# Optimization experiments

Hardware: AMD Instinct MI355X
Metric: run time of the kernel (lower is better)

Reference implementation:

```python
import jax, jax.numpy as jnp
import numpy as np

BN_EPS = 1e-5


def conv1x1(x, w, b):
    # x: [B, C, H, W], w: [O, C], b: [O]
    return jnp.einsum('bchw,oc->bohw', x, w) + b[None, :, None, None]


def cca(x, wq, bq, wk, bk, wv, bv, wg, bg):
    # Criss-cross attention block: full HWxHW attention with qk dim = C//8
    B, C, H, W = x.shape
    N = H * W
    q = conv1x1(x, wq, bq).reshape(B, -1, N)   # [B, C//8, N]
    k = conv1x1(x, wk, bk).reshape(B, -1, N)   # [B, C//8, N]
    v = conv1x1(x, wv, bv).reshape(B, C, N)    # [B, C, N]
    att = jax.nn.softmax(jnp.einsum('bdq,bdk->bqk', q, k), axis=-1)  # [B, N, N]
    out = jnp.einsum('bck,bqk->bcq', v, att).reshape(B, C, H, W)
    return x + conv1x1(out, wg, bg)


def setup_inputs() -> dict:
    key = jax.random.key(0)
    ks = iter(jax.random.split(key, 64))

    def rn(shape, s=0.1):
        return jax.random.normal(next(ks), shape, dtype=jnp.float32) * s

    C_IN = [48, 96, 192, 384]
    OC = 8            # hardcoded out_channels in the module
    NOUT = 19         # num_outputs
    LC = OC * 4       # last_inp_channels
    d = {}
    d['x0'] = rn((2, 48, 96, 96), 1.0)
    d['x1'] = rn((2, 96, 48, 48), 1.0)
    d['x2'] = rn((2, 192, 24, 24), 1.0)
    d['x3'] = rn((2, 384, 12, 12), 1.0)
    for i, c in enumerate(C_IN):
        d[f'w{i}'] = rn((OC, c))
        d[f'b{i}'] = rn((OC,))
    # cca3 params are never used by the original forward (it calls cca1 on x_3),
    # so only cca0/cca1/cca2 are materialized.
    for i in range(3):
        d[f'cca{i}_wq'] = rn((OC // 8, OC)); d[f'cca{i}_bq'] = rn((OC // 8,))
        d[f'cca{i}_wk'] = rn((OC // 8, OC)); d[f'cca{i}_bk'] = rn((OC // 8,))
        d[f'cca{i}_wv'] = rn((OC, OC));      d[f'cca{i}_bv'] = rn((OC,))
        d[f'cca{i}_wg'] = rn((OC, OC));      d[f'cca{i}_bg'] = rn((OC,))
    d['wl0'] = rn((LC, LC)); d['bl0'] = rn((LC,))
    d['bn_s'] = jnp.ones((LC,), jnp.float32)
    d['bn_b'] = jnp.zeros((LC,), jnp.float32)
    d['bn_m'] = rn((LC,), 0.01)
    d['bn_v'] = jnp.ones((LC,), jnp.float32)
    d['wl1'] = rn((NOUT, LC)); d['bl1'] = rn((NOUT,))
    return d


def reference(x0, x1, x2, x3, w0, b0, w1, b1, w2, b2, w3, b3,
              cca0_wq, cca0_bq, cca0_wk, cca0_bk, cca0_wv, cca0_bv, cca0_wg, cca0_bg,
              cca1_wq, cca1_bq, cca1_wk, cca1_bk, cca1_wv, cca1_bv, cca1_wg, cca1_bg,
              cca2_wq, cca2_bq, cca2_wk, cca2_bk, cca2_wv, cca2_bv, cca2_wg, cca2_bg,
              wl0, bl0, bn_s, bn_b, bn_m, bn_v, wl1, bl1):
    y0 = cca(conv1x1(x0, w0, b0), cca0_wq, cca0_bq, cca0_wk, cca0_bk, cca0_wv, cca0_bv, cca0_wg, cca0_bg)
    y1 = cca(conv1x1(x1, w1, b1), cca1_wq, cca1_bq, cca1_wk, cca1_bk, cca1_wv, cca1_bv, cca1_wg, cca1_bg)
    y2 = cca(conv1x1(x2, w2, b2), cca2_wq, cca2_bq, cca2_wk, cca2_bk, cca2_wv, cca2_bv, cca2_wg, cca2_bg)
    # NOTE: original torch code applies cca1 (not cca3) to x_3 -- reproduced faithfully.
    y3 = cca(conv1x1(x3, w3, b3), cca1_wq, cca1_bq, cca1_wk, cca1_bk, cca1_wv, cca1_bv, cca1_wg, cca1_bg)

    B, C, H0, W0 = y0.shape

    def up(t):
        # torch F.interpolate(mode='bilinear', align_corners=False) == jax half-pixel bilinear
        return jax.image.resize(t, (t.shape[0], t.shape[1], H0, W0), method='bilinear')

    x = jnp.concatenate([y0, up(y1), up(y2), up(y3)], axis=1)  # [B, 32, H0, W0]
    x = conv1x1(x, wl0, bl0)
    scale = (bn_s / jnp.sqrt(bn_v + BN_EPS))[None, :, None, None]
    x = (x - bn_m[None, :, None, None]) * scale + bn_b[None, :, None, None]
    x = jax.nn.relu(x)
    return conv1x1(x, wl1, bl1)
```

## Files before the change

### kernel.cpp

```cpp
#include <hip/hip_runtime.h>
#include <math.h>

#define LB __launch_bounds__(256)

#define NSLOT 24480
#define MT 28
#define NMOM 252
#define NBLK_Q 540
#define NSLICE 4

typedef float f32x4 __attribute__((ext_vector_type(4)));

struct QkvmArgs {
  const float *x0, *x1, *x2, *x3;
  const float *w0, *w1, *w2, *w3;
  const float *c0, *c1, *c2, *c3;
  const float *wq[4], *bq[4], *wk[4], *bk[4], *wv[4], *bv[4];
  float *P, *Q;
  float *MOMP;
};

template<int CG>
__device__ __forceinline__ void qkvm_body(const QkvmArgs& a, const int scale, const int C,
    const int N, const int slotoff, const int rel,
    const float* __restrict__ xp, const float* __restrict__ wp, const float* __restrict__ bp,
    float* s_w, float* s_sm, float* s_red, float* s_kp, float* s_v) {
  constexpr int PX = 256 / CG;
  const int tid = threadIdx.x;
  const int bpb = N / PX;
  const int b = rel / bpb, blk = rel - b*bpb;
  const int px = tid & (PX - 1), cg = tid / PX;
  const int n = blk*PX + px;
  const float* xb = xp + (size_t)b*C*N + n;
  const int c0 = cg*12;
  float xv[12];
  #pragma unroll
  for (int cc = 0; cc < 12; ++cc) xv[cc] = xb[(size_t)(c0+cc)*N];

  for (int i = tid; i < 8*C; i += 256) { const int c = i >> 3, o = i & 7; s_w[i] = wp[o*C + c]; }
  if (tid >= 128 && tid < 192) { const int t = tid - 128; s_sm[32 + t] = a.wv[scale][(t & 7)*8 + (t >> 3)]; }
  if (tid < 8) {
    s_sm[tid]      = bp[tid];
    s_sm[8 + tid]  = a.wq[scale][tid];
    s_sm[16 + tid] = a.wk[scale][tid];
    s_sm[24 + tid] = a.bv[scale][tid];
  }
  if (tid == 96) { s_sm[96] = a.bq[scale][0]; s_sm[97] = a.bk[scale][0]; }
  __syncthreads();

  float p[8];
  #pragma unroll
  for (int o = 0; o < 8; ++o) p[o] = 0.f;
  #pragma unroll
  for (int cc = 0; cc < 12; ++cc) {
    const float x = xv[cc];
    #pragma unroll
    for (int o = 0; o < 8; ++o) p[o] = fmaf(s_w[(c0+cc)*8+o], x, p[o]);
  }
  f32x4* sp = (f32x4*)&s_red[tid*8];
  sp[0] = (f32x4){p[0], p[1], p[2], p[3]};
  sp[1] = (f32x4){p[4], p[5], p[6], p[7]};
  __syncthreads();

  if (tid < PX) {
    float pc[8];
    #pragma unroll
    for (int o = 0; o < 8; ++o) {
      float s = s_sm[o];
      #pragma unroll
      for (int g = 0; g < CG; ++g) s += s_red[(g*PX + tid)*8 + o];
      pc[o] = s;
    }
    float q = s_sm[96], kv = s_sm[97];
    #pragma unroll
    for (int c = 0; c < 8; ++c) { q = fmaf(s_sm[8+c], pc[c], q); kv = fmaf(s_sm[16+c], pc[c], kv); }
    float v[8];
    #pragma unroll
    for (int o = 0; o < 8; ++o) v[o] = s_sm[24 + o];
    #pragma unroll
    for (int c = 0; c < 8; ++c) {
      const float pcc = pc[c];
      #pragma unroll
      for (int o = 0; o < 8; ++o) v[o] = fmaf(s_sm[32 + c*8 + o], pcc, v[o]);
    }
    const int g = slotoff + b*N + n;
    f32x4* Pp = (f32x4*)&a.P[(size_t)g*8];
    Pp[0] = (f32x4){pc[0], pc[1], pc[2], pc[3]};
    Pp[1] = (f32x4){pc[4], pc[5], pc[6], pc[7]};
    a.Q[g] = q;
    s_kp[tid*MT] = 1.f;
    float pw = 1.f;
    #pragma unroll
    for (int m = 1; m < MT; ++m) { pw *= kv; s_kp[tid*MT + m] = pw; }
    #pragma unroll
    for (int j = 0; j < 8; ++j) s_v[tid*8 + j] = v[j];
  }
  __syncthreads();

  if (tid < NMOM) {
    const int m = tid / 9, j = tid - m*9;
    float acc = 0.f;
    if (j == 0) {
      #pragma unroll 8
      for (int e = 0; e < PX; ++e) acc += s_kp[e*MT + m];
    } else {
      #pragma unroll 8
      for (int e = 0; e < PX; ++e) acc = fmaf(s_kp[e*MT + m], s_v[e*8 + (j-1)], acc);
    }
    a.MOMP[(size_t)blockIdx.x*NMOM + tid] = acc;
  }
}

__global__ LB void qkvm_kernel(QkvmArgs a) {
  __shared__ __align__(16) float s_w[3072];
  __shared__ __align__(16) float s_sm[104];
  __shared__ __align__(16) float s_red[256*8];
  __shared__ __align__(16) float s_kp[64*MT];
  __shared__ __align__(16) float s_v[64*8];
  const int bid = blockIdx.x;
  if (bid < 288)      qkvm_body<4> (a, 0, 48,  9216, 0,     bid,     a.x0, a.w0, a.c0, s_w, s_sm, s_red, s_kp, s_v);
  else if (bid < 432) qkvm_body<8> (a, 1, 96,  2304, 18432, bid-288, a.x1, a.w1, a.c1, s_w, s_sm, s_red, s_kp, s_v);
  else if (bid < 504) qkvm_body<16>(a, 2, 192, 576,  23040, bid-432, a.x2, a.w2, a.c2, s_w, s_sm, s_red, s_kp, s_v);
  else                qkvm_body<32>(a, 3, 384, 144,  24192, bid-504, a.x3, a.w3, a.c3, s_w, s_sm, s_red, s_kp, s_v);
}

__global__ LB void momred_kernel(const float* __restrict__ MOMP, float* __restrict__ MOMQ) {
  const int sb = blockIdx.x / NSLICE, sl = blockIdx.x - sb*NSLICE;
  const int tid = threadIdx.x;
  if (tid >= NMOM) return;
  const int start[8] = {0, 144, 288, 360, 432, 468, 504, 522};
  const int cnt[8]   = {144, 144, 72, 72, 36, 36, 18, 18};
  const int r0 = start[sb] + (cnt[sb]*sl)/NSLICE;
  const int r1 = start[sb] + (cnt[sb]*(sl+1))/NSLICE;
  const float* bp = MOMP + (size_t)r0*NMOM + tid;
  const int c = r1 - r0;
  float a0=0.f,a1=0.f,a2=0.f,a3=0.f,a4=0.f,a5=0.f,a6=0.f,a7=0.f;
  int t = 0;
  for (; t + 8 <= c; t += 8) {
    a0 += bp[(size_t)(t+0)*NMOM];
    a1 += bp[(size_t)(t+1)*NMOM];
    a2 += bp[(size_t)(t+2)*NMOM];
    a3 += bp[(size_t)(t+3)*NMOM];
    a4 += bp[(size_t)(t+4)*NMOM];
    a5 += bp[(size_t)(t+5)*NMOM];
    a6 += bp[(size_t)(t+6)*NMOM];
    a7 += bp[(size_t)(t+7)*NMOM];
  }
  for (; t < c; ++t) a0 += bp[(size_t)t*NMOM];
  const float s = ((a0+a1)+(a2+a3)) + ((a4+a5)+(a6+a7));
  MOMQ[(size_t)blockIdx.x*NMOM + tid] = s;
}

struct FinArgs {
  const float *Q, *P, *MOMQ;
  const float *wg0, *bg0, *wg1, *bg1, *wg2, *bg2;
  float *Y;
};

__global__ LB void finish_kernel(FinArgs a) {
  __shared__ __align__(16) float smom[8*MT*12];
  __shared__ float swg[3][64], sbg[3][8];
  const int tid = threadIdx.x;
  for (int i = tid; i < 8*MT*12; i += 256) smom[i] = 0.f;
  if (tid < 64) { swg[0][tid] = a.wg0[tid]; swg[1][tid] = a.wg1[tid]; swg[2][tid] = a.wg2[tid]; }
  if (tid < 8)  { sbg[0][tid] = a.bg0[tid]; sbg[1][tid] = a.bg1[tid]; sbg[2][tid] = a.bg2[tid]; }
  __syncthreads();
  for (int i = tid; i < 8*NMOM; i += 256) {
    const int sbi = i / NMOM, r = i - sbi*NMOM;
    const int m = r / 9, j = r - m*9;
    const float* qp = a.MOMQ + (size_t)sbi*NSLICE*NMOM + r;
    float s = 0.f;
    #pragma unroll
    for (int sl = 0; sl < NSLICE; ++sl) s += qp[(size_t)sl*NMOM];
    smom[sbi*(MT*12) + m*12 + j] = s;
  }
  __syncthreads();
  const int g = blockIdx.x*256 + tid;
  if (g >= NSLOT) return;
  int scale, N, off, widx;
  if (g < 18432)      { scale=0; N=9216; off=0;     widx=0; }
  else if (g < 23040) { scale=1; N=2304; off=18432; widx=1; }
  else if (g < 24192) { scale=2; N=576;  off=23040; widx=2; }
  else                { scale=3; N=144;  off=24192; widx=1; }
  const int b = (g - off >= N) ? 1 : 0;
  const int sb = scale*2 + b;
  const float q = a.Q[g];
  const float* mb = &smom[sb*(MT*12)];
  float t = 1.f, den = 0.f;
  float num[8];
  #pragma unroll
  for (int c = 0; c < 8; ++c) num[c] = 0.f;
  #pragma unroll
  for (int m = 0; m < MT; ++m) {
    const f32x4 a0 = *(const f32x4*)&mb[m*12];
    const f32x4 a1 = *(const f32x4*)&mb[m*12 + 4];
    const f32x4 a2 = *(const f32x4*)&mb[m*12 + 8];
    den    = fmaf(t, a0.x, den);
    num[0] = fmaf(t, a0.y, num[0]); num[1] = fmaf(t, a0.z, num[1]); num[2] = fmaf(t, a0.w, num[2]);
    num[3] = fmaf(t, a1.x, num[3]); num[4] = fmaf(t, a1.y, num[4]); num[5] = fmaf(t, a1.z, num[5]);
    num[6] = fmaf(t, a1.w, num[6]); num[7] = fmaf(t, a2.x, num[7]);
    if (m + 1 < MT) t *= q * (1.f/(float)(m+1));
  }
  const float inv = 1.f/den;
  float o8[8];
  #pragma unroll
  for (int c = 0; c < 8; ++c) o8[c] = num[c]*inv;
  const f32x4 pA = *(const f32x4*)&a.P[(size_t)g*8];
  const f32x4 pB = *(const f32x4*)&a.P[(size_t)g*8 + 4];
  const float pv[8] = {pA.x, pA.y, pA.z, pA.w, pB.x, pB.y, pB.z, pB.w};
  const float* wg = swg[widx];
  float y[8];
  #pragma unroll
  for (int o = 0; o < 8; ++o) {
    float s2 = pv[o] + sbg[widx][o];
    #pragma unroll
    for (int c = 0; c < 8; ++c) s2 = fmaf(wg[o*8 + c], o8[c], s2);
    y[o] = s2;
  }
  f32x4* Yp = (f32x4*)&a.Y[(size_t)g*8];
  Yp[0] = (f32x4){y[0], y[1], y[2], y[3]};
  Yp[1] = (f32x4){y[4], y[5], y[6], y[7]};
}

template<int HS>
__device__ inline void bilerp8(float* zo, const float* Yb, int h, int w) {
  constexpr float inv = (float)HS/96.0f;
  const float sy = (h + 0.5f)*inv - 0.5f;
  const float sx = (w + 0.5f)*inv - 0.5f;
  const int iy0 = (int)floorf(sy); const float fy = sy - (float)iy0;
  const int ix0 = (int)floorf(sx); const float fx = sx - (float)ix0;
  const int y0 = min(max(iy0, 0), HS-1), y1 = min(max(iy0 + 1, 0), HS-1);
  const int x0 = min(max(ix0, 0), HS-1), x1 = min(max(ix0 + 1, 0), HS-1);
  const float* p00 = &Yb[(size_t)(y0*HS + x0)*8];
  const float* p01 = &Yb[(size_t)(y0*HS + x1)*8];
  const float* p10 = &Yb[(size_t)(y1*HS + x0)*8];
  const float* p11 = &Yb[(size_t)(y1*HS + x1)*8];
  const float w00 = (1.f-fy)*(1.f-fx), w01 = (1.f-fy)*fx, w10 = fy*(1.f-fx), w11 = fy*fx;
  #pragma unroll
  for (int c = 0; c < 8; ++c)
    zo[c] = w00*p00[c] + w01*p01[c] + w10*p10[c] + w11*p11[c];
}

__global__ LB void head_kernel(const float* __restrict__ Y,
                               const float* wl0, const float* bl0,
                               const float* bn_s, const float* bn_b,
                               const float* bn_m, const float* bn_v,
                               const float* wl1, const float* bl1,
                               float* __restrict__ out) {
  __shared__ float s_wl0[1024], s_wl1[608];
  __shared__ float s_bl0[32], s_sc[32], s_sh[32], s_bl1[19];
  const int tid = threadIdx.x;
  for (int i = tid; i < 1024; i += 256) s_wl0[i] = wl0[i];
  for (int i = tid; i < 608;  i += 256) s_wl1[i] = wl1[i];
  if (tid < 32) {
    s_bl0[tid] = bl0[tid];
    const float sc = bn_s[tid] / sqrtf(bn_v[tid] + 1e-5f);
    s_sc[tid] = sc;
    s_sh[tid] = bn_b[tid] - bn_m[tid]*sc;
  }
  if (tid >= 32 && tid < 51) s_bl1[tid - 32] = bl1[tid - 32];
  __syncthreads();
  const int gp = blockIdx.x*256 + tid;
  const int b = (gp >= 9216) ? 1 : 0;
  const int n = gp - b*9216;
  const int h = n / 96, w = n - h*96;
  float z[32];
  {
    const float4 zA = *(const float4*)&Y[(size_t)(b*9216 + n)*8];
    const float4 zB = *(const float4*)&Y[(size_t)(b*9216 + n)*8 + 4];
    z[0]=zA.x; z[1]=zA.y; z[2]=zA.z; z[3]=zA.w; z[4]=zB.x; z[5]=zB.y; z[6]=zB.z; z[7]=zB.w;
  }
  bilerp8<48>(z + 8,  &Y[(size_t)(18432 + b*2304)*8], h, w);
  bilerp8<24>(z + 16, &Y[(size_t)(23040 + b*576)*8],  h, w);
  bilerp8<12>(z + 24, &Y[(size_t)(24192 + b*144)*8],  h, w);
  float o19[19];
  #pragma unroll
  for (int j = 0; j < 19; ++j) o19[j] = s_bl1[j];
  #pragma unroll 1
  for (int o = 0; o < 32; ++o) {
    float sA = s_bl0[o], sB = 0.f;
    #pragma unroll
    for (int c4 = 0; c4 < 4; ++c4) {
      const float4 wv = *(const float4*)&s_wl0[o*32 + c4*4];
      sA = fmaf(wv.x, z[c4*4+0], sA);
      sA = fmaf(wv.y, z[c4*4+1], sA);
      sA = fmaf(wv.z, z[c4*4+2], sA);
      sA = fmaf(wv.w, z[c4*4+3], sA);
    }
    #pragma unroll
    for (int c4 = 4; c4 < 8; ++c4) {
      const float4 wv = *(const float4*)&s_wl0[o*32 + c4*4];
      sB = fmaf(wv.x, z[c4*4+0], sB);
      sB = fmaf(wv.y, z[c4*4+1], sB);
      sB = fmaf(wv.z, z[c4*4+2], sB);
      sB = fmaf(wv.w, z[c4*4+3], sB);
    }
    const float t = fmaxf(fmaf(sA + sB, s_sc[o], s_sh[o]), 0.f);
    #pragma unroll
    for (int j = 0; j < 19; ++j) o19[j] = fmaf(s_wl1[j*32 + o], t, o19[j]);
  }
  #pragma unroll
  for (int j = 0; j < 19; ++j)
    out[((size_t)b*19 + j)*9216 + n] = o19[j];
}

extern "C" void kernel_launch(void* const* d_in, const int* in_sizes, int n_in,
                              void* d_out, int out_size, void* d_ws, size_t ws_size,
                              hipStream_t stream) {
  (void)in_sizes; (void)n_in; (void)out_size; (void)ws_size;
  const float* wq[3]; const float* bq[3]; const float* wk[3]; const float* bk[3];
  const float* wv[3]; const float* bv[3]; const float* wg[3]; const float* bg[3];
  for (int i = 0; i < 3; ++i) {
    const int base = 12 + i*8;
    wq[i] = (const float*)d_in[base + 0]; bq[i] = (const float*)d_in[base + 1];
    wk[i] = (const float*)d_in[base + 2]; bk[i] = (const float*)d_in[base + 3];
    wv[i] = (const float*)d_in[base + 4]; bv[i] = (const float*)d_in[base + 5];
    wg[i] = (const float*)d_in[base + 6]; bg[i] = (const float*)d_in[base + 7];
  }
  const int m4[4] = {0, 1, 2, 1};

  float* ws = (float*)d_ws;
  float* P = ws;
  float* Q = P + (size_t)NSLOT*8;
  float* MOMP = Q + NSLOT;
  float* MOMQ = MOMP + (size_t)NBLK_Q*NMOM;
  float* Y = MOMQ + (size_t)8*NSLICE*NMOM;

  QkvmArgs qa;
  qa.x0 = (const float*)d_in[0]; qa.x1 = (const float*)d_in[1];
  qa.x2 = (const float*)d_in[2]; qa.x3 = (const float*)d_in[3];
  qa.w0 = (const float*)d_in[4];  qa.c0 = (const float*)d_in[5];
  qa.w1 = (const float*)d_in[6];  qa.c1 = (const float*)d_in[7];
  qa.w2 = (const float*)d_in[8];  qa.c2 = (const float*)d_in[9];
  qa.w3 = (const float*)d_in[10]; qa.c3 = (const float*)d_in[11];
  for (int s = 0; s < 4; ++s) {
    qa.wq[s] = wq[m4[s]]; qa.bq[s] = bq[m4[s]];
    qa.wk[s] = wk[m4[s]]; qa.bk[s] = bk[m4[s]];
    qa.wv[s] = wv[m4[s]]; qa.bv[s] = bv[m4[s]];
  }
  qa.P = P; qa.Q = Q; qa.MOMP = MOMP;

  FinArgs fa;
  fa.Q = Q; fa.P = P; fa.MOMQ = MOMQ;
  fa.wg0 = wg[0]; fa.bg0 = bg[0];
  fa.wg1 = wg[1]; fa.bg1 = bg[1];
  fa.wg2 = wg[2]; fa.bg2 = bg[2];
  fa.Y = Y;

  qkvm_kernel<<<NBLK_Q, 256, 0, stream>>>(qa);
  momred_kernel<<<8*NSLICE, 256, 0, stream>>>(MOMP, MOMQ);
  finish_kernel<<<96, 256, 0, stream>>>(fa);
  head_kernel<<<72, 256, 0, stream>>>(Y, (const float*)d_in[36], (const float*)d_in[37],
                                      (const float*)d_in[38], (const float*)d_in[39],
                                      (const float*)d_in[40], (const float*)d_in[41],
                                      (const float*)d_in[42], (const float*)d_in[43],
                                      (float*)d_out);
}
```

Before: 32.39 us.

## Fuse attention finish and head kernels into one row-pair kernel

Merges the finish kernel (Taylor-moment attention evaluation plus gamma conv) and the head kernel (upsample, concat conv, BN, ReLU, output conv) into one launch. Each block handles two output rows of one batch. It recomputes the low-resolution rows it needs for bilinear interpolation into LDS and reads them from there instead of from a global Y buffer. This removes one kernel launch and the Y round trip through global memory. In exchange, the moment reduction and low-res Taylor evaluations are done redundantly across blocks, only 192 of 256 threads do head work, and LDS use per block is larger.

```diff
diff --git a/kernel.cpp b/kernel.cpp
--- a/kernel.cpp
+++ b/kernel.cpp
@@ -151,41 +151,9 @@
   MOMQ[(size_t)blockIdx.x*NMOM + tid] = s;
 }
 
-struct FinArgs {
-  const float *Q, *P, *MOMQ;
-  const float *wg0, *bg0, *wg1, *bg1, *wg2, *bg2;
-  float *Y;
-};
-
-__global__ LB void finish_kernel(FinArgs a) {
-  __shared__ __align__(16) float smom[8*MT*12];
-  __shared__ float swg[3][64], sbg[3][8];
-  const int tid = threadIdx.x;
-  for (int i = tid; i < 8*MT*12; i += 256) smom[i] = 0.f;
-  if (tid < 64) { swg[0][tid] = a.wg0[tid]; swg[1][tid] = a.wg1[tid]; swg[2][tid] = a.wg2[tid]; }
-  if (tid < 8)  { sbg[0][tid] = a.bg0[tid]; sbg[1][tid] = a.bg1[tid]; sbg[2][tid] = a.bg2[tid]; }
-  __syncthreads();
-  for (int i = tid; i < 8*NMOM; i += 256) {
-    const int sbi = i / NMOM, r = i - sbi*NMOM;
-    const int m = r / 9, j = r - m*9;
-    const float* qp = a.MOMQ + (size_t)sbi*NSLICE*NMOM + r;
-    float s = 0.f;
-    #pragma unroll
-    for (int sl = 0; sl < NSLICE; ++sl) s += qp[(size_t)sl*NMOM];
-    smom[sbi*(MT*12) + m*12 + j] = s;
-  }
-  __syncthreads();
-  const int g = blockIdx.x*256 + tid;
-  if (g >= NSLOT) return;
-  int scale, N, off, widx;
-  if (g < 18432)      { scale=0; N=9216; off=0;     widx=0; }
-  else if (g < 23040) { scale=1; N=2304; off=18432; widx=1; }
-  else if (g < 24192) { scale=2; N=576;  off=23040; widx=2; }
-  else                { scale=3; N=144;  off=24192; widx=1; }
-  const int b = (g - off >= N) ? 1 : 0;
-  const int sb = scale*2 + b;
-  const float q = a.Q[g];
-  const float* mb = &smom[sb*(MT*12)];
+__device__ __forceinline__ void taylor_eval(const float* __restrict__ mb, const float* __restrict__ wg,
+                                            const float* __restrict__ bg8, const float q,
+                                            const float* __restrict__ Pp, float* y) {
   float t = 1.f, den = 0.f;
   float num[8];
   #pragma unroll
@@ -205,103 +173,141 @@
   float o8[8];
   #pragma unroll
   for (int c = 0; c < 8; ++c) o8[c] = num[c]*inv;
-  const f32x4 pA = *(const f32x4*)&a.P[(size_t)g*8];
-  const f32x4 pB = *(const f32x4*)&a.P[(size_t)g*8 + 4];
+  const f32x4 pA = *(const f32x4*)Pp;
+  const f32x4 pB = *(const f32x4*)(Pp + 4);
   const float pv[8] = {pA.x, pA.y, pA.z, pA.w, pB.x, pB.y, pB.z, pB.w};
-  const float* wg = swg[widx];
-  float y[8];
   #pragma unroll
   for (int o = 0; o < 8; ++o) {
-    float s2 = pv[o] + sbg[widx][o];
+    float s2 = pv[o] + bg8[o];
     #pragma unroll
     for (int c = 0; c < 8; ++c) s2 = fmaf(wg[o*8 + c], o8[c], s2);
     y[o] = s2;
   }
-  f32x4* Yp = (f32x4*)&a.Y[(size_t)g*8];
-  Yp[0] = (f32x4){y[0], y[1], y[2], y[3]};
-  Yp[1] = (f32x4){y[4], y[5], y[6], y[7]};
 }
 
 template<int HS>
-__device__ inline void bilerp8(float* zo, const float* Yb, int h, int w) {
+__device__ __forceinline__ void bilerp_lds(float* zo, const float* __restrict__ sYb,
+                                           const int r, const int h, const int w) {
   constexpr float inv = (float)HS/96.0f;
   const float sy = (h + 0.5f)*inv - 0.5f;
   const float sx = (w + 0.5f)*inv - 0.5f;
   const int iy0 = (int)floorf(sy); const float fy = sy - (float)iy0;
   const int ix0 = (int)floorf(sx); const float fx = sx - (float)ix0;
-  const int y0 = min(max(iy0, 0), HS-1), y1 = min(max(iy0 + 1, 0), HS-1);
+  const float syE = (2*r + 0.5f)*inv - 0.5f;
+  const int ybase = (int)floorf(syE);
+  const int ly0 = iy0 - ybase;
   const int x0 = min(max(ix0, 0), HS-1), x1 = min(max(ix0 + 1, 0), HS-1);
-  const float* p00 = &Yb[(size_t)(y0*HS + x0)*8];
-  const float* p01 = &Yb[(size_t)(y0*HS + x1)*8];
-  const float* p10 = &Yb[(size_t)(y1*HS + x0)*8];
-  const float* p11 = &Yb[(size_t)(y1*HS + x1)*8];
+  const float* p00 = &sYb[((ly0  )*HS + x0)*8];
+  const float* p01 = &sYb[((ly0  )*HS + x1)*8];
+  const float* p10 = &sYb[((ly0+1)*HS + x0)*8];
+  const float* p11 = &sYb[((ly0+1)*HS + x1)*8];
   const float w00 = (1.f-fy)*(1.f-fx), w01 = (1.f-fy)*fx, w10 = fy*(1.f-fx), w11 = fy*fx;
   #pragma unroll
   for (int c = 0; c < 8; ++c)
     zo[c] = w00*p00[c] + w01*p01[c] + w10*p10[c] + w11*p11[c];
 }
 
-__global__ LB void head_kernel(const float* __restrict__ Y,
-                               const float* wl0, const float* bl0,
-                               const float* bn_s, const float* bn_b,
-                               const float* bn_m, const float* bn_v,
-                               const float* wl1, const float* bl1,
-                               float* __restrict__ out) {
+struct HFArgs {
+  const float *Q, *P, *MOMQ;
+  const float *wg0, *bg0, *wg1, *bg1, *wg2, *bg2;
+  const float *wl0, *bl0, *bn_s, *bn_b, *bn_m, *bn_v, *wl1, *bl1;
+  float *out;
+};
+
+__global__ LB void headfin_kernel(HFArgs a) {
+  __shared__ __align__(16) float smom[8*MT*12];
+  __shared__ __align__(16) float sY[2016];
+  __shared__ float swg[3][64], sbg[3][8];
   __shared__ float s_wl0[1024], s_wl1[608];
   __shared__ float s_bl0[32], s_sc[32], s_sh[32], s_bl1[19];
   const int tid = threadIdx.x;
-  for (int i = tid; i < 1024; i += 256) s_wl0[i] = wl0[i];
-  for (int i = tid; i < 608;  i += 256) s_wl1[i] = wl1[i];
-  if (tid < 32) {
-    s_bl0[tid] = bl0[tid];
-    const float sc = bn_s[tid] / sqrtf(bn_v[tid] + 1e-5f);
-    s_sc[tid] = sc;
-    s_sh[tid] = bn_b[tid] - bn_m[tid]*sc;
-  }
-  if (tid >= 32 && tid < 51) s_bl1[tid - 32] = bl1[tid - 32];
-  __syncthreads();
-  const int gp = blockIdx.x*256 + tid;
-  const int b = (gp >= 9216) ? 1 : 0;
-  const int n = gp - b*9216;
-  const int h = n / 96, w = n - h*96;
-  float z[32];
-  {
-    const float4 zA = *(const float4*)&Y[(size_t)(b*9216 + n)*8];
-    const float4 zB = *(const float4*)&Y[(size_t)(b*9216 + n)*8 + 4];
-    z[0]=zA.x; z[1]=zA.y; z[2]=zA.z; z[3]=zA.w; z[4]=zB.x; z[5]=zB.y; z[6]=zB.z; z[7]=zB.w;
-  }
-  bilerp8<48>(z + 8,  &Y[(size_t)(18432 + b*2304)*8], h, w);
-  bilerp8<24>(z + 16, &Y[(size_t)(23040 + b*576)*8],  h, w);
-  bilerp8<12>(z + 24, &Y[(size_t)(24192 + b*144)*8],  h, w);
-  float o19[19];
-  #pragma unroll
-  for (int j = 0; j < 19; ++j) o19[j] = s_bl1[j];
-  #pragma unroll 1
-  for (int o = 0; o < 32; ++o) {
-    float sA = s_bl0[o], sB = 0.f;
-    #pragma unroll
-    for (int c4 = 0; c4 < 4; ++c4) {
-      const float4 wv = *(const float4*)&s_wl0[o*32 + c4*4];
-      sA = fmaf(wv.x, z[c4*4+0], sA);
-      sA = fmaf(wv.y, z[c4*4+1], sA);
-      sA = fmaf(wv.z, z[c4*4+2], sA);
-      sA = fmaf(wv.w, z[c4*4+3], sA);
-    }
-    #pragma unroll
-    for (int c4 = 4; c4 < 8; ++c4) {
-      const float4 wv = *(const float4*)&s_wl0[o*32 + c4*4];
-      sB = fmaf(wv.x, z[c4*4+0], sB);
-      sB = fmaf(wv.y, z[c4*4+1], sB);
-      sB = fmaf(wv.z, z[c4*4+2], sB);
-      sB = fmaf(wv.w, z[c4*4+3], sB);
-    }
-    const float t = fmaxf(fmaf(sA + sB, s_sc[o], s_sh[o]), 0.f);
-    #pragma unroll
-    for (int j = 0; j < 19; ++j) o19[j] = fmaf(s_wl1[j*32 + o], t, o19[j]);
-  }
-  #pragma unroll
-  for (int j = 0; j < 19; ++j)
-    out[((size_t)b*19 + j)*9216 + n] = o19[j];
+  const int bid = blockIdx.x;
+  const int b = bid / 48, r = bid - b*48;
+
+  for (int i = tid; i < 1024; i += 256) s_wl0[i] = a.wl0[i];
+  for (int i = tid; i < 608;  i += 256) s_wl1[i] = a.wl1[i];
+  if (tid < 64) { swg[0][tid] = a.wg0[tid]; swg[1][tid] = a.wg1[tid]; swg[2][tid] = a.wg2[tid]; }
+  if (tid < 8)  { sbg[0][tid] = a.bg0[tid]; sbg[1][tid] = a.bg1[tid]; sbg[2][tid] = a.bg2[tid]; }
+  if (tid >= 64 && tid < 96) {
+    const int c = tid - 64;
+    s_bl0[c] = a.bl0[c];
+    const float sc = a.bn_s[c] / sqrtf(a.bn_v[c] + 1e-5f);
+    s_sc[c] = sc;
+    s_sh[c] = a.bn_b[c] - a.bn_m[c]*sc;
+  }
+  if (tid >= 96 && tid < 115) s_bl1[tid - 96] = a.bl1[tid - 96];
+  for (int i = tid; i < 8*MT*12; i += 256) {
+    const int sbi = i / (MT*12), rr = i - sbi*(MT*12);
+    const int m = rr / 12, j = rr - m*12;
+    float s = 0.f;
+    if (j < 9) {
+      const float* qp = a.MOMQ + (size_t)sbi*NSLICE*NMOM + (m*9 + j);
+      #pragma unroll
+      for (int sl = 0; sl < NSLICE; ++sl) s += qp[(size_t)sl*NMOM];
+    }
+    smom[i] = s;
+  }
+  __syncthreads();
+
+  if (tid < 252) {
+    int HS, soff, Nc, sb, widx, base, row_i, x;
+    if (tid < 144)      { HS=48; soff=18432; Nc=2304; sb=2+b; widx=1; base=0;    row_i=tid/48;       x=tid-48*(tid/48); }
+    else if (tid < 216) { const int t=tid-144; HS=24; soff=23040; Nc=576; sb=4+b; widx=2; base=1152; row_i=t/24; x=t-24*(t/24); }
+    else                { const int t=tid-216; HS=12; soff=24192; Nc=144; sb=6+b; widx=1; base=1728; row_i=t/12; x=t-12*(t/12); }
+    const float syE = (2*r + 0.5f)*(float)HS/96.0f - 0.5f;
+    const int ybase = (int)floorf(syE);
+    const int row = min(max(ybase + row_i, 0), HS-1);
+    const int slot = soff + b*Nc + row*HS + x;
+    float y[8];
+    taylor_eval(&smom[sb*(MT*12)], swg[widx], sbg[widx], a.Q[slot], &a.P[(size_t)slot*8], y);
+    #pragma unroll
+    for (int c = 0; c < 8; ++c) sY[base + (row_i*HS + x)*8 + c] = y[c];
+  }
+  __syncthreads();
+
+  if (tid < 192) {
+    const int hh = tid / 96;
+    const int h = 2*r + hh;
+    const int w = tid - 96*hh;
+    const int n = h*96 + w;
+    float z[32];
+    {
+      const int slot = b*9216 + n;
+      taylor_eval(&smom[b*(MT*12)], swg[0], sbg[0], a.Q[slot], &a.P[(size_t)slot*8], z);
+    }
+    bilerp_lds<48>(z + 8,  &sY[0],    r, h, w);
+    bilerp_lds<24>(z + 16, &sY[1152], r, h, w);
+    bilerp_lds<12>(z + 24, &sY[1728], r, h, w);
+    float o19[19];
+    #pragma unroll
+    for (int j = 0; j < 19; ++j) o19[j] = s_bl1[j];
+    #pragma unroll 1
+    for (int o = 0; o < 32; ++o) {
+      float sA = s_bl0[o], sB = 0.f;
+      #pragma unroll
+      for (int c4 = 0; c4 < 4; ++c4) {
+        const f32x4 wv = *(const f32x4*)&s_wl0[o*32 + c4*4];
+        sA = fmaf(wv.x, z[c4*4+0], sA);
+        sA = fmaf(wv.y, z[c4*4+1], sA);
+        sA = fmaf(wv.z, z[c4*4+2], sA);
+        sA = fmaf(wv.w, z[c4*4+3], sA);
+      }
+      #pragma unroll
+      for (int c4 = 4; c4 < 8; ++c4) {
+        const f32x4 wv = *(const f32x4*)&s_wl0[o*32 + c4*4];
+        sB = fmaf(wv.x, z[c4*4+0], sB);
+        sB = fmaf(wv.y, z[c4*4+1], sB);
+        sB = fmaf(wv.z, z[c4*4+2], sB);
+        sB = fmaf(wv.w, z[c4*4+3], sB);
+      }
+      const float t = fmaxf(fmaf(sA + sB, s_sc[o], s_sh[o]), 0.f);
+      #pragma unroll
+      for (int j = 0; j < 19; ++j) o19[j] = fmaf(s_wl1[j*32 + o], t, o19[j]);
+    }
+    #pragma unroll
+    for (int j = 0; j < 19; ++j)
+      a.out[((size_t)b*19 + j)*9216 + n] = o19[j];
+  }
 }
 
 extern "C" void kernel_launch(void* const* d_in, const int* in_sizes, int n_in,
@@ -324,7 +330,6 @@
   float* Q = P + (size_t)NSLOT*8;
   float* MOMP = Q + NSLOT;
   float* MOMQ = MOMP + (size_t)NBLK_Q*NMOM;
-  float* Y = MOMQ + (size_t)8*NSLICE*NMOM;
 
   QkvmArgs qa;
   qa.x0 = (const float*)d_in[0]; qa.x1 = (const float*)d_in[1];
@@ -340,19 +345,18 @@
   }
   qa.P = P; qa.Q = Q; qa.MOMP = MOMP;
 
-  FinArgs fa;
-  fa.Q = Q; fa.P = P; fa.MOMQ = MOMQ;
-  fa.wg0 = wg[0]; fa.bg0 = bg[0];
-  fa.wg1 = wg[1]; fa.bg1 = bg[1];
-  fa.wg2 = wg[2]; fa.bg2 = bg[2];
-  fa.Y = Y;
+  HFArgs ha;
+  ha.Q = Q; ha.P = P; ha.MOMQ = MOMQ;
+  ha.wg0 = wg[0]; ha.bg0 = bg[0];
+  ha.wg1 = wg[1]; ha.bg1 = bg[1];
+  ha.wg2 = wg[2]; ha.bg2 = bg[2];
+  ha.wl0 = (const float*)d_in[36]; ha.bl0 = (const float*)d_in[37];
+  ha.bn_s = (const float*)d_in[38]; ha.bn_b = (const float*)d_in[39];
+  ha.bn_m = (const float*)d_in[40]; ha.bn_v = (const float*)d_in[41];
+  ha.wl1 = (const float*)d_in[42]; ha.bl1 = (const float*)d_in[43];
+  ha.out = (float*)d_out;
 
   qkvm_kernel<<<NBLK_Q, 256, 0, stream>>>(qa);
   momred_kernel<<<8*NSLICE, 256, 0, stream>>>(MOMP, MOMQ);
-  finish_kernel<<<96, 256, 0, stream>>>(fa);
-  head_kernel<<<72, 256, 0, stream>>>(Y, (const float*)d_in[36], (const float*)d_in[37],
-                                      (const float*)d_in[38], (const float*)d_in[39],
-                                      (const float*)d_in[40], (const float*)d_in[41],
-                                      (const float*)d_in[42], (const float*)d_in[43],
-                                      (float*)d_out);
-}
+  headfin_kernel<<<96, 256, 0, stream>>>(ha);
+}
```

Result: no change. 32.98 us (+1.8%).
